# Performance work log

Measured on AMD Instinct MI355X. Metric: run time of the kernel, lower is better.

## Reference

```python
import jax, jax.numpy as jnp
import numpy as np
import math

B, Q, D, H = 256, 512, 32, 192
BLOCKS, KERNEL, EXPAND = 2, 9, 2
HID = H * EXPAND
IN_CH = 3 * D  # feature_mode='y_dy_ddy'


def _ln(x, w, b, eps=1e-5):
    m = x.mean(-1, keepdims=True)
    v = ((x - m) ** 2).mean(-1, keepdims=True)
    return (x - m) * jax.lax.rsqrt(v + eps) * w + b


def _features(x_in):
    # [y, dy, ddy] with dy[0]=0, ddy[0]=ddy[1 via diff]=...
    dy = jnp.concatenate([jnp.zeros_like(x_in[:, :1]), jnp.diff(x_in, axis=1)], axis=1)
    ddy = jnp.concatenate([jnp.zeros_like(dy[:, :1]), jnp.diff(dy, axis=1)], axis=1)
    return jnp.concatenate([x_in, dy, ddy], axis=-1)  # [B,Q,3D]


def _rotate(x, rho, phi):
    M = x.shape[-1] // 2
    re, im = x[:, :M], x[:, M:]
    c, s = jnp.cos(phi), jnp.sin(phi)
    return jnp.concatenate([rho * (c * re - s * im), rho * (s * re + c * im)], axis=1)


def _rho_phi(h2):
    return jax.nn.sigmoid(h2[:, 0:1]) * 1.25, math.pi * jnp.tanh(h2[:, 1:2])


def _block(h, dw_w, dw_b, ln_w, ln_b, pw1_w, pw1_b, grn_g, grn_b, pw2_w, pw2_b):
    # h: [B,C,T]; depthwise conv with replicate padding
    pad = KERNEL // 2
    y = jnp.pad(h, ((0, 0), (0, 0), (pad, pad)), mode='edge')
    y = jax.lax.conv_general_dilated(
        y, dw_w, (1,), 'VALID',
        dimension_numbers=('NCH', 'OIH', 'NCH'),
        feature_group_count=h.shape[1]) + dw_b[None, :, None]
    y = _ln(y.transpose(0, 2, 1), ln_w, ln_b).transpose(0, 2, 1)
    y = jnp.einsum('bct,oc->bot', y, pw1_w) + pw1_b[None, :, None]  # pw expand
    y = jax.nn.gelu(y, approximate=False)
    # GRN: L2 over time, normalize by channel-mean
    gx = jnp.sqrt(jnp.sum(y * y, axis=2, keepdims=True))  # [B,C,1]
    nx = gx / (gx.mean(axis=1, keepdims=True) + 1e-6)
    y = grn_g[None, :, None] * (y * nx) + grn_b[None, :, None] + y
    y = jnp.einsum('bct,oc->bot', y, pw2_w) + pw2_b[None, :, None]  # pw shrink
    return h + y  # dropout is identity in eval


def _forward(x_in, inp_w, inp_b, b_dw_w, b_dw_b, b_ln_w, b_ln_b,
             b_pw1_w, b_pw1_b, b_grn_g, b_grn_b, b_pw2_w, b_pw2_b,
             out_ln_w, out_ln_b, fc_rp_w, fc_rp_b, fc_gain_w, fc_gain_b,
             roll_in_w, roll_in_b, gru_wih, gru_whh, gru_bih, gru_bhh,
             roll_ln_w, roll_ln_b, fc_rp_r_w, fc_rp_r_b, w_out):
    feats = _features(x_in)  # [B,Q,3D]
    h = jnp.einsum('btc,oc->bot', feats, inp_w) + inp_b[None, :, None]  # [B,H,Q]
    for i in range(BLOCKS):
        h = _block(h, b_dw_w[i], b_dw_b[i], b_ln_w[i], b_ln_b[i],
                   b_pw1_w[i], b_pw1_b[i], b_grn_g[i], b_grn_b[i],
                   b_pw2_w[i], b_pw2_b[i])
    h_seq = _ln(h.transpose(0, 2, 1), out_ln_w, out_ln_b)  # [B,Q,H]

    # predict-correct Kalman loop (sequential over Q)
    def kstep(x_post, inp):
        h_t, y_t = inp
        rho, phi = _rho_phi(h_t @ fc_rp_w.T + fc_rp_b)
        x_pri = _rotate(x_post, rho, phi)
        gain = jax.nn.sigmoid(h_t @ fc_gain_w.T + fc_gain_b)
        return x_pri + gain * (y_t - x_pri), None

    x_post, _ = jax.lax.scan(
        kstep, x_in[:, 0, :],
        (h_seq.transpose(1, 0, 2), x_in.transpose(1, 0, 2)))

    # GRU rollout
    Hn = gru_whh.shape[1]

    def rstep(carry, _):
        h_r, curr = carry
        x = jnp.tanh(jnp.concatenate([h_r, curr], 1) @ roll_in_w.T + roll_in_b)
        gi = x @ gru_wih.T + gru_bih
        gh = h_r @ gru_whh.T + gru_bhh
        r = jax.nn.sigmoid(gi[:, :Hn] + gh[:, :Hn])
        z = jax.nn.sigmoid(gi[:, Hn:2 * Hn] + gh[:, Hn:2 * Hn])
        n = jnp.tanh(gi[:, 2 * Hn:] + r * gh[:, 2 * Hn:])
        h_new = _ln((1 - z) * n + z * h_r, roll_ln_w, roll_ln_b)
        rho, phi = _rho_phi(h_new @ fc_rp_r_w.T + fc_rp_r_b)
        curr_new = _rotate(curr, rho, phi)
        return (h_new, curr_new), curr_new

    _, preds = jax.lax.scan(rstep, (h_seq[:, -1, :], x_post), None, length=w_out)
    return preds.transpose(1, 0, 2)  # [B, w_out, D]


def setup_inputs() -> dict:
    key = jax.random.key(0)
    ks = jax.random.split(key, 32)
    n = lambda i, shape, s=0.05: jax.random.normal(ks[i], shape, jnp.float32) * s
    return {
        'x_in': jax.random.normal(ks[0], (B, Q, D), jnp.float32),
        'inp_w': n(1, (H, IN_CH)), 'inp_b': n(2, (H,)),
        'b_dw_w': n(3, (BLOCKS, H, 1, KERNEL)), 'b_dw_b': n(4, (BLOCKS, H)),
        'b_ln_w': 1.0 + n(5, (BLOCKS, H)), 'b_ln_b': n(6, (BLOCKS, H)),
        'b_pw1_w': n(7, (BLOCKS, HID, H)), 'b_pw1_b': n(8, (BLOCKS, HID)),
        'b_grn_g': n(9, (BLOCKS, HID)), 'b_grn_b': n(10, (BLOCKS, HID)),
        'b_pw2_w': n(11, (BLOCKS, H, HID)), 'b_pw2_b': n(12, (BLOCKS, H)),
        'out_ln_w': 1.0 + n(13, (H,)), 'out_ln_b': n(14, (H,)),
        'fc_rp_w': n(15, (2, H)), 'fc_rp_b': n(16, (2,)),
        'fc_gain_w': n(17, (D, H)), 'fc_gain_b': n(18, (D,)),
        'roll_in_w': n(19, (H, H + D)), 'roll_in_b': n(20, (H,)),
        'gru_wih': n(21, (3 * H, H)), 'gru_whh': n(22, (3 * H, H)),
        'gru_bih': n(23, (3 * H,)), 'gru_bhh': n(24, (3 * H,)),
        'roll_ln_w': 1.0 + n(25, (H,)), 'roll_ln_b': n(26, (H,)),
        'fc_rp_r_w': n(27, (2, H)), 'fc_rp_r_b': n(28, (2,)),
        'w_out': 64,
    }


def reference(x_in, inp_w, inp_b, b_dw_w, b_dw_b, b_ln_w, b_ln_b,
              b_pw1_w, b_pw1_b, b_grn_g, b_grn_b, b_pw2_w, b_pw2_b,
              out_ln_w, out_ln_b, fc_rp_w, fc_rp_b, fc_gain_w, fc_gain_b,
              roll_in_w, roll_in_b, gru_wih, gru_whh, gru_bih, gru_bhh,
              roll_ln_w, roll_ln_b, fc_rp_r_w, fc_rp_r_b, w_out):
    return _forward(x_in, inp_w, inp_b, b_dw_w, b_dw_b, b_ln_w, b_ln_b,
                    b_pw1_w, b_pw1_b, b_grn_g, b_grn_b, b_pw2_w, b_pw2_b,
                    out_ln_w, out_ln_b, fc_rp_w, fc_rp_b, fc_gain_w, fc_gain_b,
                    roll_in_w, roll_in_b, gru_wih, gru_whh, gru_bih, gru_bhh,
                    roll_ln_w, roll_ln_b, fc_rp_r_w, fc_rp_r_b, int(w_out))
```

## Files before the change

kernel.cpp:

```cpp
#include <hip/hip_runtime.h>
#include <cstdint>
#include <cstddef>

#define B_    256
#define Q_    512
#define D_    32
#define H_    192
#define HID_  384
#define INCH_ 96
#define M_    (B_*Q_)
#define WOUT_ 64
#define BPB   2
#define RT_   768
#define PI_F  3.14159265358979323846f
#define LDS_S 40

typedef unsigned int uint_t;
typedef __attribute__((ext_vector_type(8))) short short8v;
typedef __attribute__((ext_vector_type(4))) float floatx4;

__device__ __forceinline__ float sigm(float x){ return 1.f/(1.f+expf(-x)); }
__device__ __forceinline__ float gelu_exact(float x){ return 0.5f*x*(1.f+erff(x*0.7071067811865475f)); }
__device__ __forceinline__ float4 f4sub(float4 a, float4 b){
  return make_float4(a.x-b.x, a.y-b.y, a.z-b.z, a.w-b.w);
}

__device__ __forceinline__ void f2bf2(float v, unsigned short& h, unsigned short& l){
  unsigned u = __float_as_uint(v);
  unsigned rh = u + 0x7FFFu + ((u>>16)&1u);
  h = (unsigned short)(rh>>16);
  float fh = __uint_as_float(((unsigned)h)<<16);
  float lo = v - fh;
  unsigned ul = __float_as_uint(lo);
  unsigned rl = ul + 0x7FFFu + ((ul>>16)&1u);
  l = (unsigned short)(rl>>16);
}

#define MFMA_BF16(a,b,c) __builtin_amdgcn_mfma_f32_16x16x32_bf16((a),(b),(c),0,0,0)

__device__ __forceinline__ float4 feats_load(const float* __restrict__ x, int bt, int c){
  const int t = bt & 511;
  const int seg = c >> 5, d = c & 31;
  const float* xr = x + (size_t)bt*D_ + d;
  float4 x0 = *(const float4*)xr;
  if (seg == 0) return x0;
  if (t == 0) return make_float4(0.f,0.f,0.f,0.f);
  float4 x1 = *(const float4*)(xr - D_);
  float4 dy = f4sub(x0, x1);
  if (seg == 1) return dy;
  if (t == 1) return dy;
  float4 x2 = *(const float4*)(xr - 2*D_);
  float4 dym1 = f4sub(x1, x2);
  return f4sub(dy, dym1);
}

template<int MODE>
__global__ __launch_bounds__(256,2) void gemm_mfma(
    const float* __restrict__ Af,
    const float* __restrict__ W,  const float* __restrict__ bias,
    float* __restrict__ Cf,
    const float* __restrict__ scale, const float* __restrict__ grnb,
    float* __restrict__ gpart,
    int N, int K)
{
  __shared__ __align__(16) unsigned short smem[25600];
  unsigned short* Ah = smem;
  unsigned short* Al = smem + 128*LDS_S;
  unsigned short* Bh = smem + 256*LDS_S;
  unsigned short* Bl = smem + 256*LDS_S + 192*LDS_S;

  const int tid  = threadIdx.x;
  const int lane = tid & 63;
  const int wv   = tid >> 6;
  const int l15  = lane & 15;
  const int lg   = lane >> 4;
  const int bm = blockIdx.x*128, bn = blockIdx.y*192;

  floatx4 acc[2][12];
  #pragma unroll
  for (int i=0;i<2;i++)
    #pragma unroll
    for (int j=0;j<12;j++) acc[i][j] = (floatx4){0.f,0.f,0.f,0.f};

  const int arow = tid >> 1, akq = (tid & 1)*16;
  const float* gA = Af + (size_t)(bm+arow)*K;
  const float* srow = (MODE==2) ? (scale + (size_t)(bm>>9)*HID_) : nullptr;

  for (int k0=0; k0<K; k0+=32){
    #pragma unroll
    for (int i=0;i<4;i++){
      float4 v = *(const float4*)(gA + k0 + akq + 4*i);
      if (MODE==2){
        int c = k0 + akq + 4*i;
        float4 sc = *(const float4*)(srow+c);
        float4 gb = *(const float4*)(grnb+c);
        v.x = v.x*sc.x+gb.x; v.y = v.y*sc.y+gb.y;
        v.z = v.z*sc.z+gb.z; v.w = v.w*sc.w+gb.w;
      }
      unsigned short h0,h1,h2,h3,l0,l1,l2,l3;
      f2bf2(v.x,h0,l0); f2bf2(v.y,h1,l1); f2bf2(v.z,h2,l2); f2bf2(v.w,h3,l3);
      uint2 uh; uh.x = (unsigned)h0 | ((unsigned)h1<<16); uh.y = (unsigned)h2 | ((unsigned)h3<<16);
      uint2 ul; ul.x = (unsigned)l0 | ((unsigned)l1<<16); ul.y = (unsigned)l2 | ((unsigned)l3<<16);
      *(uint2*)&Ah[arow*LDS_S + akq + 4*i] = uh;
      *(uint2*)&Al[arow*LDS_S + akq + 4*i] = ul;
    }
    for (int idx = tid; idx < 384; idx += 256){
      int br = idx >> 1, bkq = (idx & 1)*16;
      const float* gb = W + (size_t)(bn+br)*K + k0 + bkq;
      #pragma unroll
      for (int i=0;i<4;i++){
        float4 v = *(const float4*)(gb + 4*i);
        unsigned short h0,h1,h2,h3,l0,l1,l2,l3;
        f2bf2(v.x,h0,l0); f2bf2(v.y,h1,l1); f2bf2(v.z,h2,l2); f2bf2(v.w,h3,l3);
        uint2 uh; uh.x = (unsigned)h0 | ((unsigned)h1<<16); uh.y = (unsigned)h2 | ((unsigned)h3<<16);
        uint2 ul; ul.x = (unsigned)l0 | ((unsigned)l1<<16); ul.y = (unsigned)l2 | ((unsigned)l3<<16);
        *(uint2*)&Bh[br*LDS_S + bkq + 4*i] = uh;
        *(uint2*)&Bl[br*LDS_S + bkq + 4*i] = ul;
      }
    }
    __syncthreads();

    const int a0off = (wv*32 + l15)*LDS_S + 8*lg;
    const int a1off = a0off + 16*LDS_S;
    short8v ah0 = *(const short8v*)&Ah[a0off];
    short8v al0 = *(const short8v*)&Al[a0off];
    short8v ah1 = *(const short8v*)&Ah[a1off];
    short8v al1 = *(const short8v*)&Al[a1off];
    #pragma unroll
    for (int ct=0; ct<12; ct++){
      const int boff = (ct*16 + l15)*LDS_S + 8*lg;
      short8v bh = *(const short8v*)&Bh[boff];
      short8v bl = *(const short8v*)&Bl[boff];
      acc[0][ct] = MFMA_BF16(ah0, bh, acc[0][ct]);
      acc[0][ct] = MFMA_BF16(ah0, bl, acc[0][ct]);
      acc[0][ct] = MFMA_BF16(al0, bh, acc[0][ct]);
      acc[1][ct] = MFMA_BF16(ah1, bh, acc[1][ct]);
      acc[1][ct] = MFMA_BF16(ah1, bl, acc[1][ct]);
      acc[1][ct] = MFMA_BF16(al1, bh, acc[1][ct]);
    }
    __syncthreads();
  }

  if (MODE==1){
    float* gq = (float*)smem;
    #pragma unroll
    for (int ct=0; ct<12; ct++){
      const int col = bn + ct*16 + l15;
      const float b = bias[col];
      float qc = 0.f;
      #pragma unroll
      for (int rt=0; rt<2; rt++){
        const int rbase = bm + wv*32 + rt*16 + lg*4;
        #pragma unroll
        for (int r=0;r<4;r++){
          float v = gelu_exact(acc[rt][ct][r] + b);
          Cf[(size_t)(rbase+r)*N + col] = v;
          qc += v*v;
        }
      }
      gq[(ct*16+l15)*16 + (wv*4+lg)] = qc;
    }
    __syncthreads();
    if (tid < 192){
      float s = 0.f;
      #pragma unroll
      for (int j=0;j<16;j++) s += gq[tid*16+j];
      const int slot = (bm>>7)&3, b = bm>>9;
      gpart[((size_t)(b*4+slot))*HID_ + bn + tid] = s;
    }
  } else {
    #pragma unroll
    for (int ct=0; ct<12; ct++){
      const int col = bn + ct*16 + l15;
      const float b = bias[col];
      #pragma unroll
      for (int rt=0; rt<2; rt++){
        const int rbase = bm + wv*32 + rt*16 + lg*4;
        #pragma unroll
        for (int r=0;r<4;r++){
          size_t off = (size_t)(rbase+r)*N + col;
          Cf[off] = Cf[off] + acc[rt][ct][r] + b;
        }
      }
    }
  }
}

__global__ __launch_bounds__(256,2) void gemm_inp_w192(
    const float* __restrict__ x,
    const float* __restrict__ W,  const float* __restrict__ bias,
    float* __restrict__ Cf)
{
  __shared__ float smem[16*128 + 16*192];
  float* AsB = smem;
  float* BsB = smem + 16*128;
  const int tid = threadIdx.x;
  const int bm = blockIdx.x*128;
  const int tx = tid & 15, ty = tid >> 4;
  const int arow = tid >> 1, ak = (tid & 1)*4;
  const int br = tid >> 2,  bk = (tid & 3)*4;
  const int K = INCH_, N = H_;

  float acc[8][12];
  #pragma unroll
  for (int i=0;i<8;i++)
    #pragma unroll
    for (int j=0;j<12;j++) acc[i][j]=0.f;

  const float* gB0 = W + (size_t)(br)*K;
  const float* gB1 = W + (size_t)(br+64)*K;
  const float* gB2 = W + (size_t)(br+128)*K;

  for (int k0=0;k0<K;k0+=16){
    float4 va0 = feats_load(x, bm+arow, k0+ak);
    float4 va1 = feats_load(x, bm+arow, k0+ak+8);
    float4 vb0 = *(const float4*)(gB0 + k0 + bk);
    float4 vb1 = *(const float4*)(gB1 + k0 + bk);
    float4 vb2 = *(const float4*)(gB2 + k0 + bk);
    AsB[(ak+0)*128+arow]=va0.x; AsB[(ak+1)*128+arow]=va0.y; AsB[(ak+2)*128+arow]=va0.z; AsB[(ak+3)*128+arow]=va0.w;
    AsB[(ak+8)*128+arow]=va1.x; AsB[(ak+9)*128+arow]=va1.y; AsB[(ak+10)*128+arow]=va1.z; AsB[(ak+11)*128+arow]=va1.w;
    BsB[(bk+0)*192+br]=vb0.x; BsB[(bk+1)*192+br]=vb0.y; BsB[(bk+2)*192+br]=vb0.z; BsB[(bk+3)*192+br]=vb0.w;
    BsB[(bk+0)*192+br+64]=vb1.x; BsB[(bk+1)*192+br+64]=vb1.y; BsB[(bk+2)*192+br+64]=vb1.z; BsB[(bk+3)*192+br+64]=vb1.w;
    BsB[(bk+0)*192+br+128]=vb2.x; BsB[(bk+1)*192+br+128]=vb2.y; BsB[(bk+2)*192+br+128]=vb2.z; BsB[(bk+3)*192+br+128]=vb2.w;
    __syncthreads();
    #pragma unroll
    for (int kk=0;kk<16;kk++){
      float4 a0 = *(const float4*)&AsB[kk*128 + ty*8];
      float4 a1 = *(const float4*)&AsB[kk*128 + ty*8 + 4];
      float4 b0 = *(const float4*)&BsB[kk*192 + tx*12];
      float4 b1 = *(const float4*)&BsB[kk*192 + tx*12 + 4];
      float4 b2 = *(const float4*)&BsB[kk*192 + tx*12 + 8];
      float ar[8] = {a0.x,a0.y,a0.z,a0.w,a1.x,a1.y,a1.z,a1.w};
      #pragma unroll
      for (int i=0;i<8;i++){
        acc[i][0] += ar[i]*b0.x; acc[i][1] += ar[i]*b0.y; acc[i][2] += ar[i]*b0.z; acc[i][3] += ar[i]*b0.w;
        acc[i][4] += ar[i]*b1.x; acc[i][5] += ar[i]*b1.y; acc[i][6] += ar[i]*b1.z; acc[i][7] += ar[i]*b1.w;
        acc[i][8] += ar[i]*b2.x; acc[i][9] += ar[i]*b2.y; acc[i][10]+= ar[i]*b2.z; acc[i][11]+= ar[i]*b2.w;
      }
    }
    __syncthreads();
  }

  const int o0 = tx*12;
  float4 bb0 = *(const float4*)(bias + o0);
  float4 bb1 = *(const float4*)(bias + o0 + 4);
  float4 bb2 = *(const float4*)(bias + o0 + 8);
  #pragma unroll
  for (int i=0;i<8;i++){
    int m = bm + ty*8 + i;
    float* crow = Cf + (size_t)m*N + o0;
    float4 v0, v1, v2;
    v0.x=acc[i][0]+bb0.x; v0.y=acc[i][1]+bb0.y; v0.z=acc[i][2]+bb0.z; v0.w=acc[i][3]+bb0.w;
    v1.x=acc[i][4]+bb1.x; v1.y=acc[i][5]+bb1.y; v1.z=acc[i][6]+bb1.z; v1.w=acc[i][7]+bb1.w;
    v2.x=acc[i][8]+bb2.x; v2.y=acc[i][9]+bb2.y; v2.z=acc[i][10]+bb2.z; v2.w=acc[i][11]+bb2.w;
    *(float4*)(crow+0) = v0; *(float4*)(crow+4) = v1; *(float4*)(crow+8) = v2;
  }
}

template<int MODE>
__global__ __launch_bounds__(256,4) void gemm_t128(
    const float* __restrict__ Af,
    const float* __restrict__ W,  const float* __restrict__ bias,
    float* __restrict__ Cf,
    const float* __restrict__ scale, const float* __restrict__ grnb,
    float* __restrict__ gpart,
    int N, int K)
{
  __shared__ float As[16][128];
  __shared__ float Bs[16][64];
  const int tid = threadIdx.x;
  const int bm = blockIdx.x*128, bn = blockIdx.y*64;
  const int tx = tid & 15, ty = tid >> 4;
  const int arow = tid >> 1, ak = (tid & 1)*4;
  const int brow = tid >> 2, bk = (tid & 3)*4;

  float acc[8][4];
  #pragma unroll
  for (int i=0;i<8;i++)
    #pragma unroll
    for (int j=0;j<4;j++) acc[i][j]=0.f;

  const float* gA = Af + (size_t)(bm+arow)*K;
  const float* gB = W  + (size_t)(bn+brow)*K;

  for (int k0=0;k0<K;k0+=16){
    float4 va0 = *(const float4*)(gA + k0 + ak);
    float4 va1 = *(const float4*)(gA + k0 + ak + 8);
    float4 vb  = *(const float4*)(gB + k0 + bk);
    As[ak+0][arow]=va0.x; As[ak+1][arow]=va0.y; As[ak+2][arow]=va0.z; As[ak+3][arow]=va0.w;
    As[ak+8][arow]=va1.x; As[ak+9][arow]=va1.y; As[ak+10][arow]=va1.z; As[ak+11][arow]=va1.w;
    Bs[bk+0][brow]=vb.x; Bs[bk+1][brow]=vb.y; Bs[bk+2][brow]=vb.z; Bs[bk+3][brow]=vb.w;
    __syncthreads();
    #pragma unroll
    for (int kk=0;kk<16;kk++){
      float4 a0 = *(const float4*)&As[kk][ty*8];
      float4 a1 = *(const float4*)&As[kk][ty*8+4];
      float4 b  = *(const float4*)&Bs[kk][tx*4];
      float ar[8] = {a0.x,a0.y,a0.z,a0.w,a1.x,a1.y,a1.z,a1.w};
      #pragma unroll
      for (int i=0;i<8;i++){
        acc[i][0] += ar[i]*b.x; acc[i][1] += ar[i]*b.y;
        acc[i][2] += ar[i]*b.z; acc[i][3] += ar[i]*b.w;
      }
    }
    __syncthreads();
  }

  const int o0 = bn + tx*4;
  float4 b0 = *(const float4*)(bias + o0);

  if (MODE==3){
    #pragma unroll
    for (int i=0;i<8;i++){
      int m = bm + ty*8 + i;
      float* ob = Cf + (size_t)m*34;
      float vx = acc[i][0]+b0.x, vy = acc[i][1]+b0.y;
      float vz = acc[i][2]+b0.z, vw = acc[i][3]+b0.w;
      if (o0 == 0){
        float rho = 1.25f*sigm(vx);
        float phi = PI_F*tanhf(vy);
        ob[0] = rho*cosf(phi); ob[1] = rho*sinf(phi);
        ob[2] = sigm(vz); ob[3] = sigm(vw);
      } else if (o0 <= 28){
        ob[o0+0]=sigm(vx); ob[o0+1]=sigm(vy); ob[o0+2]=sigm(vz); ob[o0+3]=sigm(vw);
      } else if (o0 == 32){
        ob[32]=sigm(vx); ob[33]=sigm(vy);
      }
    }
    return;
  }
  (void)gpart; (void)scale; (void)grnb;
}

__global__ __launch_bounds__(256) void dwconv_ln_wave(
  const float* __restrict__ h, const float* __restrict__ dww, const float* __restrict__ dwb,
  const float* __restrict__ lnw, const float* __restrict__ lnb, float* __restrict__ yln)
{
  __shared__ float sh[24][192];
  const int tid  = threadIdx.x;
  const int lane = tid & 63;
  const int wv   = tid >> 6;
  const int t0 = (blockIdx.x & 31) * 16;
  const size_t base = (size_t)(blockIdx.x >> 5) * Q_ * H_;
  #pragma unroll
  for (int i = tid; i < 24*192; i += 256){
    int r = i / 192, c = i - r*192;
    int tt = t0 - 4 + r; tt = tt<0?0:(tt>511?511:tt);
    sh[r][c] = h[base + (size_t)tt*H_ + c];
  }
  const int c0 = lane, c1 = lane+64, c2 = lane+128;
  float w0[9], w1[9], w2[9];
  #pragma unroll
  for (int k=0;k<9;k++){ w0[k]=dww[c0*9+k]; w1[k]=dww[c1*9+k]; w2[k]=dww[c2*9+k]; }
  const float db0=dwb[c0], db1=dwb[c1], db2=dwb[c2];
  const float lw0=lnw[c0], lw1=lnw[c1], lw2=lnw[c2];
  const float lb0=lnb[c0], lb1=lnb[c1], lb2=lnb[c2];
  __syncthreads();
  for (int it=0; it<4; it++){
    const int i = it*4 + wv;
    float a0=db0, a1=db1, a2=db2;
    #pragma unroll
    for (int k=0;k<9;k++){
      a0 += w0[k]*sh[i+k][c0];
      a1 += w1[k]*sh[i+k][c1];
      a2 += w2[k]*sh[i+k][c2];
    }
    float s = a0+a1+a2;
    float qq = a0*a0 + a1*a1 + a2*a2;
    #pragma unroll
    for (int off=32; off>0; off>>=1){ s += __shfl_down(s,off); qq += __shfl_down(qq,off); }
    s = __shfl(s, 0); qq = __shfl(qq, 0);
    float mean = s*(1.f/H_);
    float var  = qq*(1.f/H_) - mean*mean;
    float r = rsqrtf(var + 1e-5f);
    float* ob = yln + base + (size_t)(t0+i)*H_;
    ob[c0] = (a0-mean)*r*lw0 + lb0;
    ob[c1] = (a1-mean)*r*lw1 + lb1;
    ob[c2] = (a2-mean)*r*lw2 + lb2;
  }
}

__global__ __launch_bounds__(256) void out_ln_wave(
  const float* __restrict__ h, const float* __restrict__ lnw, const float* __restrict__ lnb,
  float* __restrict__ o, float* __restrict__ hlast, int b0)
{
  const int tid  = threadIdx.x;
  const int lane = tid & 63;
  const int wv   = tid >> 6;
  const int bt = blockIdx.x*4 + wv;
  const float* hr = h + (size_t)bt*H_;
  float v0 = hr[lane], v1 = hr[lane+64], v2 = hr[lane+128];
  float s = v0+v1+v2;
  float qq = v0*v0 + v1*v1 + v2*v2;
  #pragma unroll
  for (int off=32; off>0; off>>=1){ s += __shfl_down(s,off); qq += __shfl_down(qq,off); }
  s = __shfl(s, 0); qq = __shfl(qq, 0);
  float mean = s*(1.f/H_);
  float var  = qq*(1.f/H_) - mean*mean;
  float r = rsqrtf(var + 1e-5f);
  const float r0 = (v0-mean)*r*lnw[lane]     + lnb[lane];
  const float r1 = (v1-mean)*r*lnw[lane+64]  + lnb[lane+64];
  const float r2 = (v2-mean)*r*lnw[lane+128] + lnb[lane+128];
  float* orow = o + (size_t)bt*H_;
  orow[lane] = r0; orow[lane+64] = r1; orow[lane+128] = r2;
  if ((bt & 511) == 511){
    float* hl = hlast + (size_t)(b0 + (bt>>9))*H_;
    hl[lane] = r0; hl[lane+64] = r1; hl[lane+128] = r2;
  }
}

__global__ __launch_bounds__(384) void grn_combine_kernel(
  const float* __restrict__ gpart, const float* __restrict__ grn_g, float* __restrict__ scale)
{
  __shared__ float r[384];
  const int c = threadIdx.x;
  const int b = blockIdx.x;
  const float* p = gpart + (size_t)b*4*HID_;
  float s = ((p[c] + p[HID_+c]) + p[2*HID_+c]) + p[3*HID_+c];
  float gx = sqrtf(s);
  r[c] = gx;
  __syncthreads();
  if (c < 64){
    float v = r[c]+r[c+64]+r[c+128]+r[c+192]+r[c+256]+r[c+320];
    #pragma unroll
    for (int off=32; off>0; off>>=1) v += __shfl_down(v,off);
    if (c==0) r[0]=v;
  }
  __syncthreads();
  float mean = r[0]*(1.f/HID_);
  scale[(size_t)b*HID_ + c] = 1.f + grn_g[c]*gx/(mean + 1e-6f);
}

__global__ void pack_w_kernel(const float* __restrict__ frw, const float* __restrict__ frb,
                              const float* __restrict__ fgw, const float* __restrict__ fgb,
                              float* __restrict__ w_pad, float* __restrict__ b_pad)
{
  int idx = blockIdx.x*256 + threadIdx.x;
  if (idx >= 64*192) return;
  int o = idx / 192, k = idx % 192;
  float v = 0.f;
  if (o < 2) v = frw[o*192+k]; else if (o < 34) v = fgw[(o-2)*192+k];
  w_pad[idx] = v;
  if (k == 0){
    float bv = 0.f;
    if (o < 2) bv = frb[o]; else if (o < 34) bv = fgb[o-2];
    b_pad[o] = bv;
  }
}

__global__ __launch_bounds__(64) void kalman_scan_kernel(
  const float* __restrict__ x_c, const float* __restrict__ rp, float* __restrict__ xpost,
  int b0, int Bc)
{
  const int lane = threadIdx.x;
  const int bl = blockIdx.x*4 + (lane>>4);
  if (bl >= Bc) return;
  const int m = lane & 15;
  const float* xb  = x_c + (size_t)bl*Q_*D_;
  const float* rpb = rp  + (size_t)bl*Q_*34;
  float re = xb[m], im = xb[16+m];
  for (int t=0;t<Q_;t++){
    const float* r = rpb + (size_t)t*34;
    float rc = r[0], rs = r[1];
    float g0 = r[2+m], g1 = r[18+m];
    float y0 = xb[(size_t)t*D_ + m], y1v = xb[(size_t)t*D_ + 16 + m];
    float pr  = rc*re - rs*im;
    float pim = rs*re + rc*im;
    re = pr  + g0*(y0  - pr);
    im = pim + g1*(y1v - pim);
  }
  xpost[(b0+bl)*D_ + m] = re;
  xpost[(b0+bl)*D_ + 16 + m] = im;
}

__global__ void prep_rollout_kernel(const float* __restrict__ riw, const float* __restrict__ wih,
                                    const float* __restrict__ whh,
                                    float* __restrict__ wT1, float* __restrict__ wPack)
{
  int idx = blockIdx.x*256 + threadIdx.x;
  if (idx < 224*192){
    int o = idx % 192, k = idx / 192;
    wT1[idx] = riw[o*224 + k];
    return;
  }
  idx -= 224*192;
  if (idx < 192*192){
    int o = idx % 192, k = idx / 192;
    float* w = wPack + ((size_t)k*192 + o)*8;
    w[0] = wih[(0*192+o)*192 + k];
    w[1] = wih[(1*192+o)*192 + k];
    w[2] = wih[(2*192+o)*192 + k];
    w[3] = whh[(0*192+o)*192 + k];
    w[4] = whh[(1*192+o)*192 + k];
    w[5] = whh[(2*192+o)*192 + k];
    w[6] = 0.f; w[7] = 0.f;
  }
}

__global__ __launch_bounds__(RT_,3) void rollout_kernel(
  const float* __restrict__ hlast, const float* __restrict__ xpost,
  const float* __restrict__ wT1,  const float* __restrict__ rib_,
  const float* __restrict__ wPack,
  const float* __restrict__ bih,  const float* __restrict__ bhh,
  const float* __restrict__ lnw,  const float* __restrict__ lnb,
  const float* __restrict__ frw,  const float* __restrict__ frb,
  float* __restrict__ out)
{
  const int tid = threadIdx.x;
  const int q   = tid / 192;
  const int o   = tid - q*192;
  const int bb  = blockIdx.x*BPB;

  __shared__ float hT[192][2];
  __shared__ float xT[192][2];
  __shared__ float cT[32][2];
  __shared__ float pA[4][2][192];
  __shared__ float pB[4][12][192];
  __shared__ float rsum[2][3][4];

  if (q < 2){
    hT[o][q] = hlast[(size_t)(bb+q)*H_ + o];
    if (o < 32) cT[o][q] = xpost[(bb+q)*D_ + o];
  }

  const float w_ln = lnw[o], b_ln = lnb[o];
  const float fr0  = frw[o], fr1  = frw[192+o];
  const float fb0 = frb[0],  fb1 = frb[1];
  const float bi0 = bih[o], bi1 = bih[192+o], bi2 = bih[384+o];
  const float bh0 = bhh[o], bh1 = bhh[192+o], bh2 = bhh[384+o];
  const float rib = rib_[o];
  const float u0 = w_ln*fr0, u1 = w_ln*fr1;
  const float t0c = b_ln*fr0, t1c = b_ln*fr1;

  float wreg[56];
  if (q < 3){
    const int kb = 56*q;
    #pragma unroll
    for (int i=0;i<56;i++) wreg[i] = wT1[(kb+i)*192+o];
  } else {
    #pragma unroll
    for (int i=0;i<24;i++) wreg[i] = wT1[(168+i)*192+o];
    #pragma unroll
    for (int i=0;i<32;i++) wreg[24+i] = wT1[(192+i)*192+o];
  }

  {
    float c0=u0, c1=u1, k0=t0c, k1=t1c;
    #pragma unroll
    for (int off=32; off>0; off>>=1){
      c0 += __shfl_down(c0,off); c1 += __shfl_down(c1,off);
      k0 += __shfl_down(k0,off); k1 += __shfl_down(k1,off);
    }
    if (q==0 && (o&63)==0){
      int w = o>>6;
      rsum[0][w][0]=c0; rsum[0][w][1]=c1; rsum[0][w][2]=k0; rsum[0][w][3]=k1;
    }
  }
  __syncthreads();
  const float C0 = rsum[0][0][0]+rsum[0][1][0]+rsum[0][2][0];
  const float C1 = rsum[0][0][1]+rsum[0][1][1]+rsum[0][2][1];
  const float K0 = rsum[0][0][2]+rsum[0][1][2]+rsum[0][2][2] + fb0;
  const float K1 = rsum[0][0][3]+rsum[0][1][3]+rsum[0][2][3] + fb1;

  for (int s=0; s<WOUT_; s++){
    float a0=0.f, a1=0.f;
    if (q < 3){
      const int kb = 56*q;
      #pragma unroll
      for (int i=0;i<56;i++){
        float2 h2 = *(const float2*)&hT[kb+i][0];
        a0 += wreg[i]*h2.x; a1 += wreg[i]*h2.y;
      }
    } else {
      #pragma unroll
      for (int i=0;i<24;i++){
        float2 h2 = *(const float2*)&hT[168+i][0];
        a0 += wreg[i]*h2.x; a1 += wreg[i]*h2.y;
      }
      #pragma unroll
      for (int i=0;i<32;i++){
        float2 c2 = *(const float2*)&cT[i][0];
        a0 += wreg[24+i]*c2.x; a1 += wreg[24+i]*c2.y;
      }
    }
    pA[q][0][o]=a0; pA[q][1][o]=a1;
    __syncthreads();

    if (q < 2){
      xT[o][q] = tanhf(rib + pA[0][q][o] + pA[1][q][o] + pA[2][q][o] + pA[3][q][o]);
    }
    __syncthreads();

    float accx[2][3] = {{0.f,0.f,0.f},{0.f,0.f,0.f}};
    float acch[2][3] = {{0.f,0.f,0.f},{0.f,0.f,0.f}};
    {
      const int kb2 = 48*q;
      #pragma unroll 4
      for (int i=0;i<48;i++){
        const int k = kb2+i;
        const float4* wp = (const float4*)(wPack + ((size_t)k*192 + o)*8);
        const float4 wA = wp[0];
        const float4 wB = wp[1];
        const float2 xx = *(const float2*)&xT[k][0];
        const float2 hh = *(const float2*)&hT[k][0];
        accx[0][0] += wA.x*xx.x; accx[0][1] += wA.y*xx.x; accx[0][2] += wA.z*xx.x;
        accx[1][0] += wA.x*xx.y; accx[1][1] += wA.y*xx.y; accx[1][2] += wA.z*xx.y;
        acch[0][0] += wA.w*hh.x; acch[0][1] += wB.x*hh.x; acch[0][2] += wB.y*hh.x;
        acch[1][0] += wA.w*hh.y; acch[1][1] += wB.x*hh.y; acch[1][2] += wB.y*hh.y;
      }
    }
    #pragma unroll
    for (int j=0;j<2;j++){
      #pragma unroll
      for (int g=0;g<3;g++){
        pB[q][j*6+g][o]   = accx[j][g];
        pB[q][j*6+3+g][o] = acch[j][g];
      }
    }
    __syncthreads();

    float pre = 0.f;
    if (q < 2){
      const int g6 = q*6;
      float P0 = bi0 + pB[0][g6+0][o]+pB[1][g6+0][o]+pB[2][g6+0][o]+pB[3][g6+0][o];
      float P1 = bi1 + pB[0][g6+1][o]+pB[1][g6+1][o]+pB[2][g6+1][o]+pB[3][g6+1][o];
      float P2 = bi2 + pB[0][g6+2][o]+pB[1][g6+2][o]+pB[2][g6+2][o]+pB[3][g6+2][o];
      float Q0 = bh0 + pB[0][g6+3][o]+pB[1][g6+3][o]+pB[2][g6+3][o]+pB[3][g6+3][o];
      float Q1 = bh1 + pB[0][g6+4][o]+pB[1][g6+4][o]+pB[2][g6+4][o]+pB[3][g6+4][o];
      float Q2 = bh2 + pB[0][g6+5][o]+pB[1][g6+5][o]+pB[2][g6+5][o]+pB[3][g6+5][o];
      float rg = sigm(P0+Q0), zz = sigm(P1+Q1);
      float nn = tanhf(P2 + rg*Q2);
      pre = (1.f-zz)*nn + zz*hT[o][q];
      float s1 = pre, s2 = pre*pre, s3 = pre*u0, s4 = pre*u1;
      #pragma unroll
      for (int off=32; off>0; off>>=1){
        s1 += __shfl_down(s1,off); s2 += __shfl_down(s2,off);
        s3 += __shfl_down(s3,off); s4 += __shfl_down(s4,off);
      }
      if ((o&63)==0){
        int w = o>>6;
        rsum[q][w][0]=s1; rsum[q][w][1]=s2; rsum[q][w][2]=s3; rsum[q][w][3]=s4;
      }
    }
    __syncthreads();

    if (q < 2){
      float S1 = rsum[q][0][0]+rsum[q][1][0]+rsum[q][2][0];
      float S2 = rsum[q][0][1]+rsum[q][1][1]+rsum[q][2][1];
      float mu  = S1*(1.f/192.f);
      float var = S2*(1.f/192.f) - mu*mu;
      float r = rsqrtf(var+1e-5f);
      hT[o][q] = (pre-mu)*r*w_ln + b_ln;
    } else if (o < 16){
      const int j = q-2;
      float S1 = rsum[j][0][0]+rsum[j][1][0]+rsum[j][2][0];
      float S2 = rsum[j][0][1]+rsum[j][1][1]+rsum[j][2][1];
      float S3 = rsum[j][0][2]+rsum[j][1][2]+rsum[j][2][2];
      float S4 = rsum[j][0][3]+rsum[j][1][3]+rsum[j][2][3];
      float mu  = S1*(1.f/192.f);
      float var = S2*(1.f/192.f) - mu*mu;
      float r = rsqrtf(var+1e-5f);
      float proj0 = r*(S3 - mu*C0) + K0;
      float proj1 = r*(S4 - mu*C1) + K1;
      float rho = 1.25f*sigm(proj0);
      float phi = PI_F*tanhf(proj1);
      float rc = rho*cosf(phi), rs = rho*sinf(phi);
      float re = cT[o][j], im = cT[o+16][j];
      float nre = rc*re - rs*im;
      float nim = rs*re + rc*im;
      cT[o][j] = nre; cT[o+16][j] = nim;
      float* ob = out + ((size_t)(bb+j)*WOUT_ + s)*D_;
      ob[o] = nre; ob[o+16] = nim;
    }
    __syncthreads();
  }
}

extern "C" void kernel_launch(void* const* d_in, const int* in_sizes, int n_in,
                              void* d_out, int out_size, void* d_ws, size_t ws_size,
                              hipStream_t stream)
{
  const float* x_in     = (const float*)d_in[0];
  const float* inp_w    = (const float*)d_in[1];
  const float* inp_b    = (const float*)d_in[2];
  const float* b_dw_w   = (const float*)d_in[3];
  const float* b_dw_b   = (const float*)d_in[4];
  const float* b_ln_w   = (const float*)d_in[5];
  const float* b_ln_b   = (const float*)d_in[6];
  const float* b_pw1_w  = (const float*)d_in[7];
  const float* b_pw1_b  = (const float*)d_in[8];
  const float* b_grn_g  = (const float*)d_in[9];
  const float* b_grn_b  = (const float*)d_in[10];
  const float* b_pw2_w  = (const float*)d_in[11];
  const float* b_pw2_b  = (const float*)d_in[12];
  const float* out_ln_w = (const float*)d_in[13];
  const float* out_ln_b = (const float*)d_in[14];
  const float* fc_rp_w  = (const float*)d_in[15];
  const float* fc_rp_b  = (const float*)d_in[16];
  const float* fc_gain_w= (const float*)d_in[17];
  const float* fc_gain_b= (const float*)d_in[18];
  const float* roll_in_w= (const float*)d_in[19];
  const float* roll_in_b= (const float*)d_in[20];
  const float* gru_wih  = (const float*)d_in[21];
  const float* gru_whh  = (const float*)d_in[22];
  const float* gru_bih  = (const float*)d_in[23];
  const float* gru_bhh  = (const float*)d_in[24];
  const float* roll_ln_w= (const float*)d_in[25];
  const float* roll_ln_b= (const float*)d_in[26];
  const float* fc_rp_r_w= (const float*)d_in[27];
  const float* fc_rp_r_b= (const float*)d_in[28];
  float* out = (float*)d_out;

  const size_t SMAL_FLOATS = 899136 + 4096;
  size_t ws_floats = ws_size / 4;
  int nchunk = 256;
  const int cand[9] = {1,2,4,8,16,32,64,128,256};
  for (int ci=0; ci<9; ci++){
    size_t Mc_try = (size_t)M_ / cand[ci];
    if (Mc_try*768 + SMAL_FLOATS <= ws_floats){ nchunk = cand[ci]; break; }
  }
  const int    Bc = B_ / nchunk;
  const size_t Mc = (size_t)Bc * Q_;

  float* ws    = (float*)d_ws;
  float* h_c   = ws;
  float* yln_c = h_c   + Mc*192;
  float* mid_c = yln_c + Mc*192;
  float* smal  = mid_c + Mc*384;

  float* y1_c    = mid_c;
  float* rp_c    = mid_c;

  float* scaleB = smal;
  float* w_pad  = smal + 98304;
  float* b_pad  = w_pad + 12288;
  float* xpost  = b_pad + 64;
  float* hlast  = xpost + 8192;
  float* wT1    = hlast + 49152;
  float* wPack  = wT1 + 43008;
  float* gpart  = wPack + 294912;

  pack_w_kernel<<<(64*192+255)/256, 256, 0, stream>>>(fc_rp_w, fc_rp_b, fc_gain_w, fc_gain_b, w_pad, b_pad);
  prep_rollout_kernel<<<(224*192+192*192+255)/256, 256, 0, stream>>>(roll_in_w, gru_wih, gru_whh, wT1, wPack);

  const int gmx = (int)(Mc/128);
  for (int ch=0; ch<nchunk; ch++){
    const float* x_c = x_in + (size_t)ch*Mc*D_;
    gemm_inp_w192<<<dim3(gmx, 1), 256, 0, stream>>>(x_c, inp_w, inp_b, h_c);
    for (int blk = 0; blk < 2; blk++){
      const float* dww = b_dw_w + blk*H_*9;     const float* dwb = b_dw_b + blk*H_;
      const float* lnw = b_ln_w + blk*H_;       const float* lnb = b_ln_b + blk*H_;
      const float* p1w = b_pw1_w + blk*HID_*H_; const float* p1b = b_pw1_b + blk*HID_;
      const float* gg  = b_grn_g + blk*HID_;    const float* gb  = b_grn_b + blk*HID_;
      const float* p2w = b_pw2_w + blk*H_*HID_; const float* p2b = b_pw2_b + blk*H_;
      dwconv_ln_wave<<<(int)(Mc/16), 256, 0, stream>>>(h_c, dww, dwb, lnw, lnb, yln_c);
      gemm_mfma<1><<<dim3(gmx, 2), 256, 0, stream>>>(yln_c, p1w, p1b,
                                                     y1_c, nullptr, nullptr, gpart, HID_, H_);
      grn_combine_kernel<<<Bc, 384, 0, stream>>>(gpart, gg, scaleB);
      gemm_mfma<2><<<dim3(gmx, 1), 256, 0, stream>>>(y1_c, p2w, p2b,
                                                     h_c, scaleB, gb, nullptr, H_, HID_);
    }
    out_ln_wave<<<(int)(Mc/4), 256, 0, stream>>>(h_c, out_ln_w, out_ln_b, yln_c, hlast, ch*Bc);
    gemm_t128<3><<<dim3(gmx, 1), 256, 0, stream>>>(yln_c, w_pad, b_pad,
                                                   rp_c, nullptr, nullptr, nullptr, 64, H_);
    kalman_scan_kernel<<<(Bc+3)/4, 64, 0, stream>>>(x_c, rp_c, xpost, ch*Bc, Bc);
  }
  rollout_kernel<<<B_/BPB, RT_, 0, stream>>>(hlast, xpost, wT1, roll_in_b, wPack,
                                             gru_bih, gru_bhh, roll_ln_w, roll_ln_b,
                                             fc_rp_r_w, fc_rp_r_b, out);
  (void)in_sizes; (void)n_in; (void)out_size; (void)ws_size;
}
```

Before: 1.976 ms.

## Pre-split GEMM weights into bf16 hi/lo and emit packed bf16 LN output

```diff
diff --git a/kernel.cpp b/kernel.cpp
--- a/kernel.cpp
+++ b/kernel.cpp
@@ -54,10 +54,29 @@
   return f4sub(dy, dym1);
 }
 
+__global__ void prep_wbf_kernel(const float* __restrict__ w1, const float* __restrict__ w2,
+                                unsigned short* __restrict__ w1h, unsigned short* __restrict__ w1l,
+                                unsigned short* __restrict__ w2h, unsigned short* __restrict__ w2l)
+{
+  int idx = blockIdx.x*256 + threadIdx.x;
+  const int n1 = 2*HID_*H_;
+  if (idx < n1){
+    unsigned short h,l; f2bf2(w1[idx],h,l);
+    w1h[idx]=h; w1l[idx]=l;
+    return;
+  }
+  idx -= n1;
+  if (idx < 2*H_*HID_){
+    unsigned short h,l; f2bf2(w2[idx],h,l);
+    w2h[idx]=h; w2l[idx]=l;
+  }
+}
+
 template<int MODE>
 __global__ __launch_bounds__(256,2) void gemm_mfma(
-    const float* __restrict__ Af,
-    const float* __restrict__ W,  const float* __restrict__ bias,
+    const float* __restrict__ Af, const unsigned* __restrict__ Ap,
+    const unsigned short* __restrict__ Wh, const unsigned short* __restrict__ Wl,
+    const float* __restrict__ bias,
     float* __restrict__ Cf,
     const float* __restrict__ scale, const float* __restrict__ grnb,
     float* __restrict__ gpart,
@@ -83,40 +102,53 @@
     for (int j=0;j<12;j++) acc[i][j] = (floatx4){0.f,0.f,0.f,0.f};
 
   const int arow = tid >> 1, akq = (tid & 1)*16;
-  const float* gA = Af + (size_t)(bm+arow)*K;
+  const float*    gA  = (MODE==2) ? (Af + (size_t)(bm+arow)*K) : nullptr;
+  const unsigned* gAp = (MODE==1) ? (Ap + (size_t)(bm+arow)*K) : nullptr;
   const float* srow = (MODE==2) ? (scale + (size_t)(bm>>9)*HID_) : nullptr;
 
   for (int k0=0; k0<K; k0+=32){
-    #pragma unroll
-    for (int i=0;i<4;i++){
-      float4 v = *(const float4*)(gA + k0 + akq + 4*i);
-      if (MODE==2){
+    if (MODE==1){
+      #pragma unroll
+      for (int i=0;i<4;i++){
+        uint4 u = *(const uint4*)(gAp + k0 + akq + 4*i);
+        unsigned h01 = (u.x & 0xFFFFu) | (u.y << 16);
+        unsigned h23 = (u.z & 0xFFFFu) | (u.w << 16);
+        unsigned l01 = (u.x >> 16) | (u.y & 0xFFFF0000u);
+        unsigned l23 = (u.z >> 16) | (u.w & 0xFFFF0000u);
+        uint2 uh; uh.x=h01; uh.y=h23;
+        uint2 ul; ul.x=l01; ul.y=l23;
+        *(uint2*)&Ah[arow*LDS_S + akq + 4*i] = uh;
+        *(uint2*)&Al[arow*LDS_S + akq + 4*i] = ul;
+      }
+    } else {
+      #pragma unroll
+      for (int i=0;i<4;i++){
+        float4 v = *(const float4*)(gA + k0 + akq + 4*i);
         int c = k0 + akq + 4*i;
         float4 sc = *(const float4*)(srow+c);
         float4 gb = *(const float4*)(grnb+c);
         v.x = v.x*sc.x+gb.x; v.y = v.y*sc.y+gb.y;
         v.z = v.z*sc.z+gb.z; v.w = v.w*sc.w+gb.w;
-      }
-      unsigned short h0,h1,h2,h3,l0,l1,l2,l3;
-      f2bf2(v.x,h0,l0); f2bf2(v.y,h1,l1); f2bf2(v.z,h2,l2); f2bf2(v.w,h3,l3);
-      uint2 uh; uh.x = (unsigned)h0 | ((unsigned)h1<<16); uh.y = (unsigned)h2 | ((unsigned)h3<<16);
-      uint2 ul; ul.x = (unsigned)l0 | ((unsigned)l1<<16); ul.y = (unsigned)l2 | ((unsigned)l3<<16);
-      *(uint2*)&Ah[arow*LDS_S + akq + 4*i] = uh;
-      *(uint2*)&Al[arow*LDS_S + akq + 4*i] = ul;
-    }
-    for (int idx = tid; idx < 384; idx += 256){
-      int br = idx >> 1, bkq = (idx & 1)*16;
-      const float* gb = W + (size_t)(bn+br)*K + k0 + bkq;
-      #pragma unroll
-      for (int i=0;i<4;i++){
-        float4 v = *(const float4*)(gb + 4*i);
         unsigned short h0,h1,h2,h3,l0,l1,l2,l3;
         f2bf2(v.x,h0,l0); f2bf2(v.y,h1,l1); f2bf2(v.z,h2,l2); f2bf2(v.w,h3,l3);
         uint2 uh; uh.x = (unsigned)h0 | ((unsigned)h1<<16); uh.y = (unsigned)h2 | ((unsigned)h3<<16);
         uint2 ul; ul.x = (unsigned)l0 | ((unsigned)l1<<16); ul.y = (unsigned)l2 | ((unsigned)l3<<16);
-        *(uint2*)&Bh[br*LDS_S + bkq + 4*i] = uh;
-        *(uint2*)&Bl[br*LDS_S + bkq + 4*i] = ul;
-      }
+        *(uint2*)&Ah[arow*LDS_S + akq + 4*i] = uh;
+        *(uint2*)&Al[arow*LDS_S + akq + 4*i] = ul;
+      }
+    }
+    for (int idx = tid; idx < 384; idx += 256){
+      int br = idx >> 1, bkq = (idx & 1)*16;
+      const unsigned short* gh = Wh + (size_t)(bn+br)*K + k0 + bkq;
+      const unsigned short* gl = Wl + (size_t)(bn+br)*K + k0 + bkq;
+      uint4 vh0 = *(const uint4*)(gh);
+      uint4 vh1 = *(const uint4*)(gh+8);
+      uint4 vl0 = *(const uint4*)(gl);
+      uint4 vl1 = *(const uint4*)(gl+8);
+      *(uint4*)&Bh[br*LDS_S + bkq]     = vh0;
+      *(uint4*)&Bh[br*LDS_S + bkq + 8] = vh1;
+      *(uint4*)&Bl[br*LDS_S + bkq]     = vl0;
+      *(uint4*)&Bl[br*LDS_S + bkq + 8] = vl1;
     }
     __syncthreads();
 
@@ -334,7 +366,7 @@
 
 __global__ __launch_bounds__(256) void dwconv_ln_wave(
   const float* __restrict__ h, const float* __restrict__ dww, const float* __restrict__ dwb,
-  const float* __restrict__ lnw, const float* __restrict__ lnb, float* __restrict__ yln)
+  const float* __restrict__ lnw, const float* __restrict__ lnb, unsigned* __restrict__ yln)
 {
   __shared__ float sh[24][192];
   const int tid  = threadIdx.x;
@@ -373,10 +405,11 @@
     float mean = s*(1.f/H_);
     float var  = qq*(1.f/H_) - mean*mean;
     float r = rsqrtf(var + 1e-5f);
-    float* ob = yln + base + (size_t)(t0+i)*H_;
-    ob[c0] = (a0-mean)*r*lw0 + lb0;
-    ob[c1] = (a1-mean)*r*lw1 + lb1;
-    ob[c2] = (a2-mean)*r*lw2 + lb2;
+    unsigned* ob = yln + base + (size_t)(t0+i)*H_;
+    unsigned short hh,ll;
+    f2bf2((a0-mean)*r*lw0 + lb0, hh, ll); ob[c0] = (unsigned)hh | ((unsigned)ll<<16);
+    f2bf2((a1-mean)*r*lw1 + lb1, hh, ll); ob[c1] = (unsigned)hh | ((unsigned)ll<<16);
+    f2bf2((a2-mean)*r*lw2 + lb2, hh, ll); ob[c2] = (unsigned)hh | ((unsigned)ll<<16);
   }
 }
 
@@ -486,14 +519,13 @@
   idx -= 224*192;
   if (idx < 192*192){
     int o = idx % 192, k = idx / 192;
-    float* w = wPack + ((size_t)k*192 + o)*8;
+    float* w = wPack + ((size_t)(k>>1)*192 + o)*12 + (k&1)*6;
     w[0] = wih[(0*192+o)*192 + k];
     w[1] = wih[(1*192+o)*192 + k];
     w[2] = wih[(2*192+o)*192 + k];
     w[3] = whh[(0*192+o)*192 + k];
     w[4] = whh[(1*192+o)*192 + k];
     w[5] = whh[(2*192+o)*192 + k];
-    w[6] = 0.f; w[7] = 0.f;
   }
 }
 
@@ -594,19 +626,24 @@
     float accx[2][3] = {{0.f,0.f,0.f},{0.f,0.f,0.f}};
     float acch[2][3] = {{0.f,0.f,0.f},{0.f,0.f,0.f}};
     {
-      const int kb2 = 48*q;
-      #pragma unroll 4
-      for (int i=0;i<48;i++){
-        const int k = kb2+i;
-        const float4* wp = (const float4*)(wPack + ((size_t)k*192 + o)*8);
-        const float4 wA = wp[0];
-        const float4 wB = wp[1];
-        const float2 xx = *(const float2*)&xT[k][0];
-        const float2 hh = *(const float2*)&hT[k][0];
-        accx[0][0] += wA.x*xx.x; accx[0][1] += wA.y*xx.x; accx[0][2] += wA.z*xx.x;
-        accx[1][0] += wA.x*xx.y; accx[1][1] += wA.y*xx.y; accx[1][2] += wA.z*xx.y;
-        acch[0][0] += wA.w*hh.x; acch[0][1] += wB.x*hh.x; acch[0][2] += wB.y*hh.x;
-        acch[1][0] += wA.w*hh.y; acch[1][1] += wB.x*hh.y; acch[1][2] += wB.y*hh.y;
+      const int pb = 24*q;
+      #pragma unroll 2
+      for (int i=0;i<24;i++){
+        const int p = pb+i;
+        const float4* wp = (const float4*)(wPack + ((size_t)p*192 + o)*12);
+        const float4 qa = wp[0];
+        const float4 qb = wp[1];
+        const float4 qc = wp[2];
+        const float4 xx = *(const float4*)&xT[2*p][0];
+        const float4 hh = *(const float4*)&hT[2*p][0];
+        accx[0][0] += qa.x*xx.x; accx[0][1] += qa.y*xx.x; accx[0][2] += qa.z*xx.x;
+        accx[1][0] += qa.x*xx.y; accx[1][1] += qa.y*xx.y; accx[1][2] += qa.z*xx.y;
+        acch[0][0] += qa.w*hh.x; acch[0][1] += qb.x*hh.x; acch[0][2] += qb.y*hh.x;
+        acch[1][0] += qa.w*hh.y; acch[1][1] += qb.x*hh.y; acch[1][2] += qb.y*hh.y;
+        accx[0][0] += qb.z*xx.z; accx[0][1] += qb.w*xx.z; accx[0][2] += qc.x*xx.z;
+        accx[1][0] += qb.z*xx.w; accx[1][1] += qb.w*xx.w; accx[1][2] += qc.x*xx.w;
+        acch[0][0] += qc.y*hh.z; acch[0][1] += qc.z*hh.z; acch[0][2] += qc.w*hh.z;
+        acch[1][0] += qc.y*hh.w; acch[1][1] += qc.z*hh.w; acch[1][2] += qc.w*hh.w;
       }
     }
     #pragma unroll
@@ -711,7 +748,7 @@
   const float* fc_rp_r_b= (const float*)d_in[28];
   float* out = (float*)d_out;
 
-  const size_t SMAL_FLOATS = 899136 + 4096;
+  const size_t SMAL_FLOATS = 1194048 + 4096;
   size_t ws_floats = ws_size / 4;
   int nchunk = 256;
   const int cand[9] = {1,2,4,8,16,32,64,128,256};
@@ -739,9 +776,15 @@
   float* wT1    = hlast + 49152;
   float* wPack  = wT1 + 43008;
   float* gpart  = wPack + 294912;
+  float* wbf    = gpart + 393216;
+  unsigned short* w1h = (unsigned short*)wbf;
+  unsigned short* w1l = w1h + 2*HID_*H_;
+  unsigned short* w2h = w1l + 2*HID_*H_;
+  unsigned short* w2l = w2h + 2*H_*HID_;
 
   pack_w_kernel<<<(64*192+255)/256, 256, 0, stream>>>(fc_rp_w, fc_rp_b, fc_gain_w, fc_gain_b, w_pad, b_pad);
   prep_rollout_kernel<<<(224*192+192*192+255)/256, 256, 0, stream>>>(roll_in_w, gru_wih, gru_whh, wT1, wPack);
+  prep_wbf_kernel<<<(4*HID_*H_+255)/256, 256, 0, stream>>>(b_pw1_w, b_pw2_w, w1h, w1l, w2h, w2l);
 
   const int gmx = (int)(Mc/128);
   for (int ch=0; ch<nchunk; ch++){
@@ -750,14 +793,16 @@
     for (int blk = 0; blk < 2; blk++){
       const float* dww = b_dw_w + blk*H_*9;     const float* dwb = b_dw_b + blk*H_;
       const float* lnw = b_ln_w + blk*H_;       const float* lnb = b_ln_b + blk*H_;
-      const float* p1w = b_pw1_w + blk*HID_*H_; const float* p1b = b_pw1_b + blk*HID_;
+      const float* p1b = b_pw1_b + blk*HID_;
       const float* gg  = b_grn_g + blk*HID_;    const float* gb  = b_grn_b + blk*HID_;
-      const float* p2w = b_pw2_w + blk*H_*HID_; const float* p2b = b_pw2_b + blk*H_;
-      dwconv_ln_wave<<<(int)(Mc/16), 256, 0, stream>>>(h_c, dww, dwb, lnw, lnb, yln_c);
-      gemm_mfma<1><<<dim3(gmx, 2), 256, 0, stream>>>(yln_c, p1w, p1b,
+      const float* p2b = b_pw2_b + blk*H_;
+      dwconv_ln_wave<<<(int)(Mc/16), 256, 0, stream>>>(h_c, dww, dwb, lnw, lnb, (unsigned*)yln_c);
+      gemm_mfma<1><<<dim3(gmx, 2), 256, 0, stream>>>(nullptr, (const unsigned*)yln_c,
+                                                     w1h + blk*HID_*H_, w1l + blk*HID_*H_, p1b,
                                                      y1_c, nullptr, nullptr, gpart, HID_, H_);
       grn_combine_kernel<<<Bc, 384, 0, stream>>>(gpart, gg, scaleB);
-      gemm_mfma<2><<<dim3(gmx, 1), 256, 0, stream>>>(y1_c, p2w, p2b,
+      gemm_mfma<2><<<dim3(gmx, 1), 256, 0, stream>>>(y1_c, nullptr,
+                                                     w2h + blk*H_*HID_, w2l + blk*H_*HID_, p2b,
                                                      h_c, scaleB, gb, nullptr, H_, HID_);
     }
     out_ln_wave<<<(int)(Mc/4), 256, 0, stream>>>(h_c, out_ln_w, out_ln_b, yln_c, hlast, ch*Bc);
```

After: 1.889 ms (median of 2 runs). 1.05x faster.
